# Kernel optimization log

Measured on AMD Instinct MI355X. Metric: run time of the kernel, lower is better.

The kernel has to match this reference:

```python
import jax, jax.numpy as jnp
import numpy as np

N_HEAD = 16
D_MODEL = 1024
B, C = 4, 2048

def setup_inputs() -> dict:
    key = jax.random.key(0)
    k_x, k_wq, k_bq, k_wo, k_bo = jax.random.split(key, 5)
    s = 0.02
    return {
        "x": jax.random.normal(k_x, (B, C, D_MODEL), dtype=jnp.float32),
        "W_qkv": jax.random.normal(k_wq, (D_MODEL, 3 * D_MODEL), dtype=jnp.float32) * s,
        "b_qkv": jax.random.normal(k_bq, (3 * D_MODEL,), dtype=jnp.float32) * s,
        "W_o": jax.random.normal(k_wo, (D_MODEL, D_MODEL), dtype=jnp.float32) * s,
        "b_o": jax.random.normal(k_bo, (D_MODEL,), dtype=jnp.float32) * s,
    }

def reference(x, W_qkv, b_qkv, W_o, b_o):
    Bsz, Cq, D = x.shape
    H = N_HEAD
    hd = D // H
    qkv = x @ W_qkv + b_qkv                      # [B,C,3D]
    Q, K, V = jnp.split(qkv, 3, axis=2)
    # [B,C,H,hd] -> [B,H,C,hd]
    Q = Q.reshape(Bsz, Cq, H, hd).transpose(0, 2, 1, 3)
    K = K.reshape(Bsz, Cq, H, hd).transpose(0, 2, 1, 3)
    V = V.reshape(Bsz, Cq, H, hd).transpose(0, 2, 1, 3)
    scale = 1.0 / np.sqrt(hd).astype(np.float32)
    att = jnp.einsum('bhqd,bhkd->bhqk', Q, K) * scale
    causal = jnp.tril(jnp.ones((Cq, Cq), dtype=bool))
    att = jnp.where(causal, att, jnp.float32(-jnp.inf))
    att = jax.nn.softmax(att, axis=-1)           # dropout = identity (eval)
    out = jnp.einsum('bhqk,bhkd->bhqd', att, V)  # [B,H,C,hd]
    out = out.transpose(0, 2, 1, 3).reshape(Bsz, Cq, D)
    return out @ W_o + b_o
```

## Files before the change

### kernel.cpp

```cpp
#include <hip/hip_runtime.h>
#include <hip/hip_bf16.h>

typedef __attribute__((ext_vector_type(8))) short bf16x8;
typedef __attribute__((ext_vector_type(4))) float f32x4;

#define NH 16
#define DM 1024
#define HD 64
#define CSEQ 2048
#define MROWS 8192
#define NBH 64

static __device__ __forceinline__ unsigned short f2bf(float f) {
  __hip_bfloat16 h = __float2bfloat16(f);
  return *reinterpret_cast<unsigned short*>(&h);
}

static __device__ __forceinline__ short bf_qscale(short s) {
  unsigned u = ((unsigned)(unsigned short)s) << 16;
  float f = __builtin_bit_cast(float, u) * 0.18033688f;
  return (short)f2bf(f);
}

static __device__ __forceinline__ void gload_lds16(const void* g, void* l) {
  __builtin_amdgcn_global_load_lds(
      (const __attribute__((address_space(1))) unsigned int*)g,
      (__attribute__((address_space(3))) unsigned int*)l, 16, 0, 0);
}

__global__ __launch_bounds__(256) void cast_f32_bf16(const float* __restrict__ in,
                                                     unsigned short* __restrict__ out,
                                                     int n4) {
  int stride = gridDim.x * blockDim.x;
  for (int i = blockIdx.x * blockDim.x + threadIdx.x; i < n4; i += stride) {
    float4 v = ((const float4*)in)[i];
    ushort4 o;
    o.x = f2bf(v.x); o.y = f2bf(v.y); o.z = f2bf(v.z); o.w = f2bf(v.w);
    ((ushort4*)out)[i] = o;
  }
}

__global__ __launch_bounds__(256) void transpose_cast(const float* __restrict__ src,
                                                      unsigned short* __restrict__ dst,
                                                      int K, int N) {
  __shared__ float tile[32][33];
  int tx = threadIdx.x, ty = threadIdx.y;
  int n0 = blockIdx.x * 32, k0 = blockIdx.y * 32;
  #pragma unroll
  for (int i = 0; i < 32; i += 8)
    tile[ty + i][tx] = src[(size_t)(k0 + ty + i) * N + n0 + tx];
  __syncthreads();
  #pragma unroll
  for (int i = 0; i < 32; i += 8)
    dst[(size_t)(n0 + ty + i) * K + k0 + tx] = f2bf(tile[tx][ty + i]);
}

template<int CNT>
static __device__ __forceinline__ void ld_frags(const char* base, int r0, int cx, int g,
                                                bf16x8 (*out)[2]) {
  #pragma unroll
  for (int i = 0; i < CNT; i++) {
    int row = r0 + i * 16 + cx;
    #pragma unroll
    for (int kc = 0; kc < 2; kc++)
      out[i][kc] = *(const bf16x8*)(base + row * 128 + ((((kc << 2) | g) ^ (row & 7)) << 4));
  }
}

#define BARR() __builtin_amdgcn_s_barrier()
#define LGKM0() asm volatile("s_waitcnt lgkmcnt(0)" ::: "memory")
#define VMCNT8() asm volatile("s_waitcnt vmcnt(8)" ::: "memory")
#define VMCNT0() asm volatile("s_waitcnt vmcnt(0)" ::: "memory")
#define PRIO1() __builtin_amdgcn_s_setprio(1)
#define PRIO0() __builtin_amdgcn_s_setprio(0)

static __device__ __forceinline__ void mfma_all(const bf16x8 af[4][2], const bf16x8 bfr[4][2],
                                                f32x4 acc[4][4]) {
  #pragma unroll
  for (int kc = 0; kc < 2; kc++)
    #pragma unroll
    for (int mi = 0; mi < 4; mi++)
      #pragma unroll
      for (int ni = 0; ni < 4; ni++)
        acc[mi][ni] = __builtin_amdgcn_mfma_f32_16x16x32_bf16(
            af[mi][kc], bfr[ni][kc], acc[mi][ni], 0, 0, 0);
}

template<int MODE>
__global__ __launch_bounds__(256, 2) void gemm128d(const unsigned short* __restrict__ A,
                                                   const unsigned short* __restrict__ BT,
                                                   const float* __restrict__ bias,
                                                   float* __restrict__ outF,
                                                   unsigned short* __restrict__ outQKV,
                                                   int N, int K) {
  __shared__ char sA[2][16384];
  __shared__ char sB[2][16384];
  int tid = threadIdx.x;
  int w = tid >> 6, l = tid & 63, g = l >> 4, cx = l & 15;
  int wm = (w >> 1) * 64, wn = (w & 1) * 64;

  int nwgx = gridDim.x;
  int nwg = nwgx * gridDim.y;
  int gid = blockIdx.y * nwgx + blockIdx.x;
  int swz = (gid & 7) * (nwg >> 3) + (gid >> 3);
  int bm = (swz / nwgx) * 128, bn = (swz % nwgx) * 128;

  const unsigned short* Ap[4];
  const unsigned short* Bp[4];
  #pragma unroll
  for (int i = 0; i < 4; i++) {
    int c = tid + i * 256;
    int ar = c >> 3, as = ((c & 7) ^ (ar & 7)) * 8;
    Ap[i] = A + (size_t)(bm + ar) * K + as;
    Bp[i] = BT + (size_t)(bn + ar) * K + as;
  }

  #define STAGE_AB(t, buf) do { int ko_ = (t) << 6;                 \
      gload_lds16(Ap[0] + ko_, sA[buf] + (tid)       * 16);         \
      gload_lds16(Ap[1] + ko_, sA[buf] + (tid + 256) * 16);         \
      gload_lds16(Ap[2] + ko_, sA[buf] + (tid + 512) * 16);         \
      gload_lds16(Ap[3] + ko_, sA[buf] + (tid + 768) * 16);         \
      gload_lds16(Bp[0] + ko_, sB[buf] + (tid)       * 16);         \
      gload_lds16(Bp[1] + ko_, sB[buf] + (tid + 256) * 16);         \
      gload_lds16(Bp[2] + ko_, sB[buf] + (tid + 512) * 16);         \
      gload_lds16(Bp[3] + ko_, sB[buf] + (tid + 768) * 16);         \
    } while (0)

  f32x4 acc[4][4];
  #pragma unroll
  for (int i = 0; i < 4; i++)
    #pragma unroll
    for (int j = 0; j < 4; j++) acc[i][j] = (f32x4){0.f, 0.f, 0.f, 0.f};

  int NT = K >> 6;

  STAGE_AB(0, 0);
  STAGE_AB(1, 1);
  VMCNT8();
  BARR();

  int cur = 0;
  for (int t = 0; t < NT; t++) {
    const char* Ac = sA[cur];
    const char* Bc = sB[cur];
    bool h1 = (t + 1) < NT, h2 = (t + 2) < NT;
    bf16x8 af[4][2], bfr[4][2];

    ld_frags<4>(Ac, wm, cx, g, af);
    ld_frags<4>(Bc, wn, cx, g, bfr);
    LGKM0();
    BARR();

    if (h2) STAGE_AB(t + 2, cur);

    PRIO1(); mfma_all(af, bfr, acc); PRIO0();

    if (h2)      { VMCNT8(); }
    else if (h1) { VMCNT0(); }
    BARR();
    cur ^= 1;
  }

  #pragma unroll
  for (int mi = 0; mi < 4; mi++) {
    #pragma unroll
    for (int ni = 0; ni < 4; ni++) {
      int col = bn + wn + ni * 16 + cx;
      float bv = bias[col];
      int row0 = bm + wm + mi * 16 + g * 4;
      #pragma unroll
      for (int r = 0; r < 4; r++) {
        float v = acc[mi][ni][r] + bv;
        int rr = row0 + r;
        if (MODE == 0) {
          outF[(size_t)rr * N + col] = v;
        } else {
          int which = col >> 10, rem = col & 1023;
          int h = rem >> 6, d = rem & 63;
          int b = rr >> 11, cq = rr & 2047;
          if (which == 2) {
            int pos = (cq & ~31) + (((cq >> 2) & 3) << 3) + (((cq >> 4) & 1) << 2) + (cq & 3);
            outQKV[((size_t)2 * NBH + b * NH + h) * (CSEQ * HD) +
                   (size_t)d * CSEQ + pos] = f2bf(v);
          } else {
            outQKV[((size_t)which * NBH + b * NH + h) * (CSEQ * HD) + (size_t)cq * HD + d] = f2bf(v);
          }
        }
      }
    }
  }
  #undef STAGE_AB
}

__global__ __launch_bounds__(512, 4) void attn_kernel(const unsigned short* __restrict__ Qb,
                                                      const unsigned short* __restrict__ Kb,
                                                      const unsigned short* __restrict__ VTb,
                                                      unsigned short* __restrict__ O) {
  __shared__ char sKb[2][16384];
  __shared__ char sVt[2][16384];
  int tid = threadIdx.x;
  int w = tid >> 6, l = tid & 63, g = l >> 4, cx = l & 15;
  int gid = blockIdx.x;
  int bh = ((gid >> 7) << 3) | (gid & 7);
  int qt = 15 - ((gid >> 3) & 15);

  const unsigned short* Qp  = Qb  + (size_t)bh * CSEQ * HD;
  const unsigned short* Kp  = Kb  + (size_t)bh * CSEQ * HD;
  const unsigned short* VTp = VTb + (size_t)bh * CSEQ * HD;

  int qrow = qt * 128 + w * 16 + cx;
  bf16x8 qf[2];
  qf[0] = *(const bf16x8*)(Qp + (size_t)qrow * HD + g * 8);
  qf[1] = *(const bf16x8*)(Qp + (size_t)qrow * HD + 32 + g * 8);
  #pragma unroll
  for (int kc = 0; kc < 2; kc++)
    #pragma unroll
    for (int j = 0; j < 8; j++) qf[kc][j] = bf_qscale(qf[kc][j]);

  bf16x8 vones;
  #pragma unroll
  for (int j = 0; j < 8; j++) vones[j] = (short)0x3F80;

  f32x4 o[4], osum;
  #pragma unroll
  for (int nf2 = 0; nf2 < 4; nf2++) o[nf2] = (f32x4){0.f, 0.f, 0.f, 0.f};
  osum = (f32x4){0.f, 0.f, 0.f, 0.f};
  float mrow = -INFINITY;

  int c0 = tid, c1 = tid + 512;
  int krow0 = c0 >> 3, ksl0 = (c0 & 7) ^ (krow0 & 7);
  int krow1 = c1 >> 3, ksl1 = (c1 & 7) ^ (krow1 & 7);
  int vd0 = c0 >> 4, vsl0 = (c0 & 15) ^ (vd0 & 7);
  int vd1 = c1 >> 4, vsl1 = (c1 & 15) ^ (vd1 & 7);
  const unsigned short* Ksrc0 = Kp + (size_t)krow0 * HD + ksl0 * 8;
  const unsigned short* Ksrc1 = Kp + (size_t)krow1 * HD + ksl1 * 8;
  const unsigned short* Vsrc0 = VTp + (size_t)vd0 * CSEQ + vsl0 * 8;
  const unsigned short* Vsrc1 = VTp + (size_t)vd1 * CSEQ + vsl1 * 8;

  gload_lds16(Ksrc0, sKb[0] + c0 * 16);
  gload_lds16(Ksrc1, sKb[0] + c1 * 16);
  gload_lds16(Vsrc0, sVt[0] + c0 * 16);
  gload_lds16(Vsrc1, sVt[0] + c1 * 16);
  __syncthreads();
  int cur = 0;

  for (int kt = 0; kt <= qt; kt++) {
    if (kt < qt) {
      size_t ko = (size_t)(kt + 1) * 128 * HD;
      size_t vo = (size_t)(kt + 1) * 128;
      gload_lds16(Ksrc0 + ko, sKb[cur ^ 1] + c0 * 16);
      gload_lds16(Ksrc1 + ko, sKb[cur ^ 1] + c1 * 16);
      gload_lds16(Vsrc0 + vo, sVt[cur ^ 1] + c0 * 16);
      gload_lds16(Vsrc1 + vo, sVt[cur ^ 1] + c1 * 16);
    }
    const char* Kc = sKb[cur];
    const char* Vc = sVt[cur];

    f32x4 sacc[8];
    #pragma unroll
    for (int nf = 0; nf < 8; nf++) sacc[nf] = (f32x4){0.f, 0.f, 0.f, 0.f};
    __builtin_amdgcn_s_setprio(1);
    #pragma unroll
    for (int kc = 0; kc < 2; kc++) {
      #pragma unroll
      for (int nf = 0; nf < 8; nf++) {
        int row = nf * 16 + cx;
        bf16x8 kf = *(const bf16x8*)(Kc + row * 128 + ((((kc << 2) | g) ^ (row & 7)) << 4));
        sacc[nf] = __builtin_amdgcn_mfma_f32_16x16x32_bf16(kf, qf[kc], sacc[nf], 0, 0, 0);
      }
    }
    __builtin_amdgcn_s_setprio(0);

    if (kt == qt) {
      #pragma unroll
      for (int nf = 0; nf < 8; nf++)
        #pragma unroll
        for (int r = 0; r < 4; r++)
          if (nf * 16 + 4 * g + r > w * 16 + cx) sacc[nf][r] = -INFINITY;
    }
    float m8[8];
    #pragma unroll
    for (int nf = 0; nf < 8; nf++)
      m8[nf] = fmaxf(fmaxf(sacc[nf][0], sacc[nf][1]), fmaxf(sacc[nf][2], sacc[nf][3]));
    float mx = fmaxf(fmaxf(fmaxf(m8[0], m8[1]), fmaxf(m8[2], m8[3])),
                     fmaxf(fmaxf(m8[4], m8[5]), fmaxf(m8[6], m8[7])));
    mx = fmaxf(mx, __shfl_xor(mx, 16));
    mx = fmaxf(mx, __shfl_xor(mx, 32));

    if (!__all(mx - mrow <= 8.f)) {
      float mnew = fmaxf(mrow, mx);
      float alpha = __builtin_amdgcn_exp2f(mrow - mnew);
      mrow = mnew;
      #pragma unroll
      for (int r = 0; r < 4; r++) {
        float ar = __shfl(alpha, (l & 48) | ((l >> 2) & 12) | r);
        #pragma unroll
        for (int nf2 = 0; nf2 < 4; nf2++) o[nf2][r] *= ar;
        osum[r] *= ar;
      }
    }
    #pragma unroll
    for (int nf = 0; nf < 8; nf++)
      #pragma unroll
      for (int r = 0; r < 4; r++)
        sacc[nf][r] = __builtin_amdgcn_exp2f(sacc[nf][r] - mrow);

    bf16x8 pa[4];
    #pragma unroll
    for (int kc = 0; kc < 4; kc++) {
      #pragma unroll
      for (int j = 0; j < 4; j++) {
        pa[kc][j]     = (short)f2bf(sacc[2 * kc][j]);
        pa[kc][j + 4] = (short)f2bf(sacc[2 * kc + 1][j]);
      }
    }

    __builtin_amdgcn_s_setprio(1);
    #pragma unroll
    for (int kc = 0; kc < 4; kc++) {
      #pragma unroll
      for (int nf2 = 0; nf2 < 4; nf2++) {
        int d = nf2 * 16 + cx;
        bf16x8 vf = *(const bf16x8*)(Vc + ((d * 256 + (((kc << 2) | g) << 4)) ^ ((d & 7) << 4)));
        o[nf2] = __builtin_amdgcn_mfma_f32_16x16x32_bf16(pa[kc], vf, o[nf2], 0, 0, 0);
      }
      osum = __builtin_amdgcn_mfma_f32_16x16x32_bf16(pa[kc], vones, osum, 0, 0, 0);
    }
    __builtin_amdgcn_s_setprio(0);

    if (kt < qt) {
      __syncthreads();
      cur ^= 1;
    }
  }

  int b = bh >> 4, h = bh & 15;
  #pragma unroll
  for (int r = 0; r < 4; r++) {
    float inv = 1.0f / osum[r];
    int q = qt * 128 + w * 16 + 4 * g + r;
    size_t base = ((size_t)(b * CSEQ + q)) * DM + h * HD;
    #pragma unroll
    for (int nf2 = 0; nf2 < 4; nf2++)
      O[base + nf2 * 16 + cx] = f2bf(o[nf2][r] * inv);
  }
}

extern "C" void kernel_launch(void* const* d_in, const int* in_sizes, int n_in,
                              void* d_out, int out_size, void* d_ws, size_t ws_size,
                              hipStream_t stream) {
  const float* x    = (const float*)d_in[0];
  const float* Wqkv = (const float*)d_in[1];
  const float* bqkv = (const float*)d_in[2];
  const float* Wo   = (const float*)d_in[3];
  const float* bo   = (const float*)d_in[4];
  float* out = (float*)d_out;

  unsigned short* ws = (unsigned short*)d_ws;
  const size_t XB_OFF    = 0;
  const size_t WQKVT_OFF = 8388608;
  const size_t WOT_OFF   = WQKVT_OFF + 3145728;
  const size_t QKV_OFF   = WOT_OFF + 1048576;
  const size_t ATT_OFF   = QKV_OFF + 3 * 8388608;

  unsigned short* xb    = ws + XB_OFF;
  unsigned short* wqkvT = ws + WQKVT_OFF;
  unsigned short* woT   = ws + WOT_OFF;
  unsigned short* qkv   = ws + QKV_OFF;
  unsigned short* att   = ws + ATT_OFF;

  cast_f32_bf16<<<2048, 256, 0, stream>>>(x, xb, (MROWS * DM) / 4);
  transpose_cast<<<dim3(3 * DM / 32, DM / 32), dim3(32, 8), 0, stream>>>(Wqkv, wqkvT, DM, 3 * DM);
  transpose_cast<<<dim3(DM / 32, DM / 32), dim3(32, 8), 0, stream>>>(Wo, woT, DM, DM);

  gemm128d<1><<<dim3(3 * DM / 128, MROWS / 128), 256, 0, stream>>>(
      xb, wqkvT, bqkv, nullptr, qkv, 3 * DM, DM);

  attn_kernel<<<dim3(1024), 512, 0, stream>>>(
      qkv, qkv + 8388608, qkv + 16777216, att);

  gemm128d<0><<<dim3(DM / 128, MROWS / 128), 256, 0, stream>>>(
      att, woT, bo, out, nullptr, DM, DM);
}
```

Measured before the change: 190.4 us.

## Restructure attention around 32x32x16 MFMA with 256-row query tiles

The attention kernel moves from 16x16x32 MFMA tiles covering 128 query rows per block to 32x32x16 MFMA tiles where each of 8 waves owns 32 query rows, giving 256 rows per block and half as many blocks. Each K/V tile loaded into LDS now serves twice as many queries. The row sum is computed with VALU reductions instead of an extra ones-vector MFMA. P is packed to bf16 with v_cvt_pk_bf16_f32 and rearranged across lanes with shuffles to match the 32x32 operand layout, so the V-transpose write in the QKV GEMM no longer needs its position permutation. Risks are more cross-lane shuffle and VALU work per tile, higher register pressure, and coarser load balancing with fewer, larger causal blocks.

```diff
diff --git a/kernel.cpp b/kernel.cpp
--- a/kernel.cpp
+++ b/kernel.cpp
@@ -3,6 +3,8 @@
 
 typedef __attribute__((ext_vector_type(8))) short bf16x8;
 typedef __attribute__((ext_vector_type(4))) float f32x4;
+typedef __attribute__((ext_vector_type(16))) float f32x16;
+typedef __attribute__((ext_vector_type(4))) unsigned int u32x4;
 
 #define NH 16
 #define DM 1024
@@ -179,9 +181,8 @@
           int h = rem >> 6, d = rem & 63;
           int b = rr >> 11, cq = rr & 2047;
           if (which == 2) {
-            int pos = (cq & ~31) + (((cq >> 2) & 3) << 3) + (((cq >> 4) & 1) << 2) + (cq & 3);
             outQKV[((size_t)2 * NBH + b * NH + h) * (CSEQ * HD) +
-                   (size_t)d * CSEQ + pos] = f2bf(v);
+                   (size_t)d * CSEQ + cq] = f2bf(v);
           } else {
             outQKV[((size_t)which * NBH + b * NH + h) * (CSEQ * HD) + (size_t)cq * HD + d] = f2bf(v);
           }
@@ -199,33 +200,33 @@
   __shared__ char sKb[2][16384];
   __shared__ char sVt[2][16384];
   int tid = threadIdx.x;
-  int w = tid >> 6, l = tid & 63, g = l >> 4, cx = l & 15;
+  int w = tid >> 6, l = tid & 63;
+  int hi = l >> 5, lq = l & 31;
   int gid = blockIdx.x;
-  int bh = ((gid >> 7) << 3) | (gid & 7);
-  int qt = 15 - ((gid >> 3) & 15);
+  int bh = ((gid >> 6) << 3) | (gid & 7);
+  int qs = (gid >> 3) & 7;
+  int qb = (gid & 256) ? qs : (7 - qs);
+  int NKV = 2 * qb + 2;
 
   const unsigned short* Qp  = Qb  + (size_t)bh * CSEQ * HD;
   const unsigned short* Kp  = Kb  + (size_t)bh * CSEQ * HD;
   const unsigned short* VTp = VTb + (size_t)bh * CSEQ * HD;
 
-  int qrow = qt * 128 + w * 16 + cx;
-  bf16x8 qf[2];
-  qf[0] = *(const bf16x8*)(Qp + (size_t)qrow * HD + g * 8);
-  qf[1] = *(const bf16x8*)(Qp + (size_t)qrow * HD + 32 + g * 8);
-  #pragma unroll
-  for (int kc = 0; kc < 2; kc++)
-    #pragma unroll
-    for (int j = 0; j < 8; j++) qf[kc][j] = bf_qscale(qf[kc][j]);
-
-  bf16x8 vones;
-  #pragma unroll
-  for (int j = 0; j < 8; j++) vones[j] = (short)0x3F80;
-
-  f32x4 o[4], osum;
-  #pragma unroll
-  for (int nf2 = 0; nf2 < 4; nf2++) o[nf2] = (f32x4){0.f, 0.f, 0.f, 0.f};
-  osum = (f32x4){0.f, 0.f, 0.f, 0.f};
-  float mrow = -INFINITY;
+  int qglob = qb * 256 + w * 32 + lq;
+  bf16x8 qf[4];
+  #pragma unroll
+  for (int ks = 0; ks < 4; ks++) {
+    qf[ks] = *(const bf16x8*)(Qp + (size_t)qglob * HD + ks * 16 + hi * 8);
+    #pragma unroll
+    for (int j = 0; j < 8; j++) qf[ks][j] = bf_qscale(qf[ks][j]);
+  }
+
+  f32x16 o[2];
+  #pragma unroll
+  for (int dt = 0; dt < 2; dt++)
+    #pragma unroll
+    for (int e = 0; e < 16; e++) o[dt][e] = 0.f;
+  float mrow = -INFINITY, lrow = 0.f;
 
   int c0 = tid, c1 = tid + 512;
   int krow0 = c0 >> 3, ksl0 = (c0 & 7) ^ (krow0 & 7);
@@ -244,8 +245,8 @@
   __syncthreads();
   int cur = 0;
 
-  for (int kt = 0; kt <= qt; kt++) {
-    if (kt < qt) {
+  for (int kt = 0; kt < NKV; kt++) {
+    if (kt + 1 < NKV) {
       size_t ko = (size_t)(kt + 1) * 128 * HD;
       size_t vo = (size_t)(kt + 1) * 128;
       gload_lds16(Ksrc0 + ko, sKb[cur ^ 1] + c0 * 16);
@@ -256,93 +257,119 @@
     const char* Kc = sKb[cur];
     const char* Vc = sVt[cur];
 
-    f32x4 sacc[8];
-    #pragma unroll
-    for (int nf = 0; nf < 8; nf++) sacc[nf] = (f32x4){0.f, 0.f, 0.f, 0.f};
-    __builtin_amdgcn_s_setprio(1);
-    #pragma unroll
-    for (int kc = 0; kc < 2; kc++) {
-      #pragma unroll
-      for (int nf = 0; nf < 8; nf++) {
-        int row = nf * 16 + cx;
-        bf16x8 kf = *(const bf16x8*)(Kc + row * 128 + ((((kc << 2) | g) ^ (row & 7)) << 4));
-        sacc[nf] = __builtin_amdgcn_mfma_f32_16x16x32_bf16(kf, qf[kc], sacc[nf], 0, 0, 0);
+    #pragma unroll
+    for (int h = 0; h < 2; h++) {
+      f32x16 sacc[2];
+      #pragma unroll
+      for (int mt = 0; mt < 2; mt++)
+        #pragma unroll
+        for (int e = 0; e < 16; e++) sacc[mt][e] = 0.f;
+      PRIO1();
+      #pragma unroll
+      for (int ks = 0; ks < 4; ks++) {
+        #pragma unroll
+        for (int mt = 0; mt < 2; mt++) {
+          int row = h * 64 + mt * 32 + lq;
+          bf16x8 kf = *(const bf16x8*)(Kc + row * 128 + ((((ks << 1) | hi) ^ (row & 7)) << 4));
+          sacc[mt] = __builtin_amdgcn_mfma_f32_32x32x16_bf16(kf, qf[ks], sacc[mt], 0, 0, 0);
+        }
       }
+      PRIO0();
+
+      if (kt >= NKV - 2) {
+        #pragma unroll
+        for (int mt = 0; mt < 2; mt++)
+          #pragma unroll
+          for (int e = 0; e < 16; e++) {
+            int kvg = kt * 128 + h * 64 + mt * 32 + (e & 3) + 8 * (e >> 2) + 4 * hi;
+            if (kvg > qglob) sacc[mt][e] = -INFINITY;
+          }
+      }
+
+      float t16[16];
+      #pragma unroll
+      for (int e = 0; e < 16; e++) t16[e] = fmaxf(sacc[0][e], sacc[1][e]);
+      #pragma unroll
+      for (int s = 8; s >= 1; s >>= 1)
+        #pragma unroll
+        for (int i = 0; i < 8; i++) if (i < s) t16[i] = fmaxf(t16[i], t16[i + s]);
+      float mx = fmaxf(t16[0], __shfl_xor(t16[0], 32));
+
+      if (!__all(mx - mrow <= 8.f)) {
+        float mnew = fmaxf(mrow, mx);
+        float alpha = __builtin_amdgcn_exp2f(mrow - mnew);
+        mrow = mnew;
+        lrow *= alpha;
+        #pragma unroll
+        for (int e = 0; e < 16; e++) {
+          float ar = __shfl(alpha, (e & 3) + 8 * (e >> 2) + 4 * hi);
+          o[0][e] *= ar;
+          o[1][e] *= ar;
+        }
+      }
+      #pragma unroll
+      for (int mt = 0; mt < 2; mt++)
+        #pragma unroll
+        for (int e = 0; e < 16; e++)
+          sacc[mt][e] = __builtin_amdgcn_exp2f(sacc[mt][e] - mrow);
+      float s16[16];
+      #pragma unroll
+      for (int e = 0; e < 16; e++) s16[e] = sacc[0][e] + sacc[1][e];
+      #pragma unroll
+      for (int s = 8; s >= 1; s >>= 1)
+        #pragma unroll
+        for (int i = 0; i < 8; i++) if (i < s) s16[i] += s16[i + s];
+      lrow += s16[0];
+
+      PRIO1();
+      #pragma unroll
+      for (int mt = 0; mt < 2; mt++) {
+        #pragma unroll
+        for (int b2 = 0; b2 < 2; b2++) {
+          unsigned pA, pB, pC, pD;
+          asm("v_cvt_pk_bf16_f32 %0, %1, %2" : "=v"(pA) : "v"(sacc[mt][8 * b2 + 0]), "v"(sacc[mt][8 * b2 + 1]));
+          asm("v_cvt_pk_bf16_f32 %0, %1, %2" : "=v"(pB) : "v"(sacc[mt][8 * b2 + 2]), "v"(sacc[mt][8 * b2 + 3]));
+          asm("v_cvt_pk_bf16_f32 %0, %1, %2" : "=v"(pC) : "v"(sacc[mt][8 * b2 + 4]), "v"(sacc[mt][8 * b2 + 5]));
+          asm("v_cvt_pk_bf16_f32 %0, %1, %2" : "=v"(pD) : "v"(sacc[mt][8 * b2 + 6]), "v"(sacc[mt][8 * b2 + 7]));
+          unsigned tA = (unsigned)__shfl_xor((int)pA, 32);
+          unsigned tB = (unsigned)__shfl_xor((int)pB, 32);
+          unsigned tC = (unsigned)__shfl_xor((int)pC, 32);
+          unsigned tD = (unsigned)__shfl_xor((int)pD, 32);
+          u32x4 wd;
+          wd.x = hi ? tC : pA;
+          wd.y = hi ? tD : pB;
+          wd.z = hi ? pC : tA;
+          wd.w = hi ? pD : tB;
+          bf16x8 pf = __builtin_bit_cast(bf16x8, wd);
+          int slotb = h * 8 + mt * 4 + b2 * 2 + hi;
+          #pragma unroll
+          for (int dt = 0; dt < 2; dt++) {
+            int d = dt * 32 + lq;
+            bf16x8 vf = *(const bf16x8*)(Vc + ((d * 256 + slotb * 16) ^ ((d & 7) << 4)));
+            o[dt] = __builtin_amdgcn_mfma_f32_32x32x16_bf16(pf, vf, o[dt], 0, 0, 0);
+          }
+        }
+      }
+      PRIO0();
     }
-    __builtin_amdgcn_s_setprio(0);
-
-    if (kt == qt) {
-      #pragma unroll
-      for (int nf = 0; nf < 8; nf++)
-        #pragma unroll
-        for (int r = 0; r < 4; r++)
-          if (nf * 16 + 4 * g + r > w * 16 + cx) sacc[nf][r] = -INFINITY;
-    }
-    float m8[8];
-    #pragma unroll
-    for (int nf = 0; nf < 8; nf++)
-      m8[nf] = fmaxf(fmaxf(sacc[nf][0], sacc[nf][1]), fmaxf(sacc[nf][2], sacc[nf][3]));
-    float mx = fmaxf(fmaxf(fmaxf(m8[0], m8[1]), fmaxf(m8[2], m8[3])),
-                     fmaxf(fmaxf(m8[4], m8[5]), fmaxf(m8[6], m8[7])));
-    mx = fmaxf(mx, __shfl_xor(mx, 16));
-    mx = fmaxf(mx, __shfl_xor(mx, 32));
-
-    if (!__all(mx - mrow <= 8.f)) {
-      float mnew = fmaxf(mrow, mx);
-      float alpha = __builtin_amdgcn_exp2f(mrow - mnew);
-      mrow = mnew;
-      #pragma unroll
-      for (int r = 0; r < 4; r++) {
-        float ar = __shfl(alpha, (l & 48) | ((l >> 2) & 12) | r);
-        #pragma unroll
-        for (int nf2 = 0; nf2 < 4; nf2++) o[nf2][r] *= ar;
-        osum[r] *= ar;
-      }
-    }
-    #pragma unroll
-    for (int nf = 0; nf < 8; nf++)
-      #pragma unroll
-      for (int r = 0; r < 4; r++)
-        sacc[nf][r] = __builtin_amdgcn_exp2f(sacc[nf][r] - mrow);
-
-    bf16x8 pa[4];
-    #pragma unroll
-    for (int kc = 0; kc < 4; kc++) {
-      #pragma unroll
-      for (int j = 0; j < 4; j++) {
-        pa[kc][j]     = (short)f2bf(sacc[2 * kc][j]);
-        pa[kc][j + 4] = (short)f2bf(sacc[2 * kc + 1][j]);
-      }
-    }
-
-    __builtin_amdgcn_s_setprio(1);
-    #pragma unroll
-    for (int kc = 0; kc < 4; kc++) {
-      #pragma unroll
-      for (int nf2 = 0; nf2 < 4; nf2++) {
-        int d = nf2 * 16 + cx;
-        bf16x8 vf = *(const bf16x8*)(Vc + ((d * 256 + (((kc << 2) | g) << 4)) ^ ((d & 7) << 4)));
-        o[nf2] = __builtin_amdgcn_mfma_f32_16x16x32_bf16(pa[kc], vf, o[nf2], 0, 0, 0);
-      }
-      osum = __builtin_amdgcn_mfma_f32_16x16x32_bf16(pa[kc], vones, osum, 0, 0, 0);
-    }
-    __builtin_amdgcn_s_setprio(0);
-
-    if (kt < qt) {
+
+    if (kt + 1 < NKV) {
       __syncthreads();
       cur ^= 1;
     }
   }
 
-  int b = bh >> 4, h = bh & 15;
-  #pragma unroll
-  for (int r = 0; r < 4; r++) {
-    float inv = 1.0f / osum[r];
-    int q = qt * 128 + w * 16 + 4 * g + r;
-    size_t base = ((size_t)(b * CSEQ + q)) * DM + h * HD;
-    #pragma unroll
-    for (int nf2 = 0; nf2 < 4; nf2++)
-      O[base + nf2 * 16 + cx] = f2bf(o[nf2][r] * inv);
+  lrow += __shfl_xor(lrow, 32);
+  float linv = 1.0f / lrow;
+  int b = bh >> 4, hh = bh & 15;
+  #pragma unroll
+  for (int e = 0; e < 16; e++) {
+    int qloc = (e & 3) + 8 * (e >> 2) + 4 * hi;
+    float inv = __shfl(linv, qloc);
+    int q = qb * 256 + w * 32 + qloc;
+    size_t base = ((size_t)(b * CSEQ + q)) * DM + hh * HD;
+    O[base + lq]      = f2bf(o[0][e] * inv);
+    O[base + 32 + lq] = f2bf(o[1][e] * inv);
   }
 }
 
@@ -376,7 +403,7 @@
   gemm128d<1><<<dim3(3 * DM / 128, MROWS / 128), 256, 0, stream>>>(
       xb, wqkvT, bqkv, nullptr, qkv, 3 * DM, DM);
 
-  attn_kernel<<<dim3(1024), 512, 0, stream>>>(
+  attn_kernel<<<dim3(512), 512, 0, stream>>>(
       qkv, qkv + 8388608, qkv + 16777216, att);
 
   gemm128d<0><<<dim3(DM / 128, MROWS / 128), 256, 0, stream>>>(
```

After: 247.9 us. 1.3x slower.
